# Kernel optimization log

Measured on AMD Instinct MI355X. Metric: run time of the kernel, lower is better.

The kernel has to match this reference:

```python
import jax, jax.numpy as jnp
import numpy as np

B, L, D, T, S, K = 16, 4095, 768, 768, 64, 8
H = T // 2  # per-direction GRU hidden


def setup_inputs() -> dict:
    key = jax.random.key(0)
    ks = jax.random.split(key, 16)
    sc = 0.05
    hidden = jax.random.normal(ks[0], (B, L, D), jnp.float32)
    attn_len = jax.random.randint(ks[1], (B,), L // 2, L).astype(jnp.int32)
    span_start = jax.random.randint(ks[2], (B, S), 0, L - 16).astype(jnp.int32)
    span_len = jax.random.randint(ks[3], (B, S), 1, 9).astype(jnp.int32)
    return dict(
        hidden=hidden,
        W_ih_f=jax.random.normal(ks[4], (3 * H, D)) * sc,
        W_hh_f=jax.random.normal(ks[5], (3 * H, H)) * sc,
        b_ih_f=jax.random.normal(ks[6], (3 * H,)) * sc,
        b_hh_f=jax.random.normal(ks[7], (3 * H,)) * sc,
        W_ih_b=jax.random.normal(ks[8], (3 * H, D)) * sc,
        W_hh_b=jax.random.normal(ks[9], (3 * H, H)) * sc,
        b_ih_b=jax.random.normal(ks[10], (3 * H,)) * sc,
        b_hh_b=jax.random.normal(ks[11], (3 * H,)) * sc,
        W_ctx=jax.random.normal(ks[12], (T, D)) * sc,
        b_ctx=jax.random.normal(ks[13], (T,)) * sc,
        W_find=jax.random.normal(ks[14], (1, 2 * T)) * sc,
        attn_len=attn_len,
        span_start=span_start,
        span_len=span_len,
    )


def _gru_dir(x, W_ih, W_hh, b_ih, b_hh, reverse):
    # x: [B, S, D] -> [B, S, H]; torch GRU gate order: r, z, n
    def step(h, xt):
        gi = xt @ W_ih.T + b_ih            # [B, 3H]
        gh = h @ W_hh.T + b_hh
        ir, iz, inn = jnp.split(gi, 3, axis=-1)
        hr, hz, hn = jnp.split(gh, 3, axis=-1)
        r = jax.nn.sigmoid(ir + hr)
        z = jax.nn.sigmoid(iz + hz)
        n = jnp.tanh(inn + r * hn)
        h_new = (1.0 - z) * n + z * h
        return h_new, h_new
    xs = jnp.swapaxes(x, 0, 1)             # [S, B, D]
    h0 = jnp.zeros((x.shape[0], W_hh.shape[1]), x.dtype)
    _, ys = jax.lax.scan(step, h0, xs, reverse=reverse)
    return jnp.swapaxes(ys, 0, 1)          # [B, S, H]


def reference(hidden, W_ih_f, W_hh_f, b_ih_f, b_hh_f, W_ih_b, W_hh_b, b_ih_b, b_hh_b,
              W_ctx, b_ctx, W_find, attn_len, span_start, span_len):
    pos = jnp.arange(L)
    # --- per-span mean pooling (ragged spans, vectorized via masks) ---
    end = span_start + span_len - 1        # inclusive end, as hidden[start:end+1]
    mask = (pos[None, None, :] >= span_start[..., None]) & (pos[None, None, :] <= end[..., None])
    maskf = mask.astype(hidden.dtype)      # [B, S, L]
    cnt = maskf.sum(-1, keepdims=True)
    span_rep = jnp.einsum('bsl,bld->bsd', maskf, hidden) / cnt   # [B, S, D]
    # --- bidirectional GRU over the span sequence ---
    h_f = _gru_dir(span_rep, W_ih_f, W_hh_f, b_ih_f, b_hh_f, reverse=False)
    h_b = _gru_dir(span_rep, W_ih_b, W_hh_b, b_ih_b, b_hh_b, reverse=True)
    rep_ac = jnp.concatenate([h_f, h_b], axis=-1)                # [B, S, T]
    # --- context: mean over valid tokens excluding the last valid token, then linear ---
    n_ctx = (attn_len - 1).astype(hidden.dtype)                  # [B]
    ctx_mask = (pos[None, :] < (attn_len - 1)[:, None]).astype(hidden.dtype)
    ctx = jnp.einsum('bl,bld->bd', ctx_mask, hidden) / n_ctx[:, None]
    rep_context = ctx @ W_ctx.T + b_ctx                          # [B, T]
    # --- findm attention: concat + linear(no bias) + sigmoid + topk + gather ---
    all_reps = jnp.concatenate([rep_ac, rep_context[:, None, :]], axis=1)  # [B, S+1, T]
    wq, wk = W_find[0, :T], W_find[0, T:]
    # sigmoid(W [q; k]) = sigmoid(q.wq + k.wk)
    score = jax.nn.sigmoid((rep_ac @ wq)[:, :, None] + (all_reps @ wk)[:, None, :])  # [B, S, S+1]
    vals, idx = jax.lax.top_k(score, K)                          # [B, S, K]
    v1 = jnp.take_along_axis(all_reps[:, None, :, :], idx[..., None], axis=2)        # [B, S, K, T]
    return rep_ac, rep_context, v1, vals, idx
```

## Files before the change

kernel.cpp:

```cpp
#include <hip/hip_runtime.h>
#include <hip/hip_bf16.h>
#include <math.h>

#define BB 16
#define LL 4095
#define DD 768
#define TT 768
#define SS 64
#define KK 8
#define HH 384
#define G3 1152
#define NWPD 24

__global__ void span_mean_kernel(const float* __restrict__ hidden,
                                 const int* __restrict__ sstart,
                                 const int* __restrict__ slen,
                                 float* __restrict__ span) {
    int bs = blockIdx.x;
    int b = bs >> 6;
    int st = sstart[bs];
    int ln = slen[bs];
    const float* base = hidden + ((size_t)b * LL + st) * DD;
    float inv = 1.0f / (float)ln;
    for (int d = threadIdx.x; d < DD; d += 256) {
        float acc = 0.0f;
        for (int r = 0; r < ln; ++r) acc += base[(size_t)r * DD + d];
        span[(size_t)bs * DD + d] = acc * inv;
    }
}

__global__ void ctx_accum_kernel(const float* __restrict__ hidden,
                                 const int* __restrict__ attn_len,
                                 float* __restrict__ ctx) {
    int b = blockIdx.x, chunk = blockIdx.y;
    int lim = attn_len[b] - 1;
    int l0 = chunk * 128;
    int l1 = min(l0 + 128, lim);
    if (l0 >= l1) return;
    int t = threadIdx.x;
    const float* base = hidden + (size_t)b * LL * DD;
    float a0 = 0.f, a1 = 0.f, a2 = 0.f;
    for (int l = l0; l < l1; ++l) {
        const float* row = base + (size_t)l * DD;
        a0 += row[t]; a1 += row[t + 256]; a2 += row[t + 512];
    }
    atomicAdd(&ctx[b * DD + t], a0);
    atomicAdd(&ctx[b * DD + t + 256], a1);
    atomicAdd(&ctx[b * DD + t + 512], a2);
}

__global__ void repctx_kernel(const float* __restrict__ ctxsum,
                              const int* __restrict__ attn_len,
                              const float* __restrict__ W_ctx,
                              const float* __restrict__ b_ctx,
                              float* __restrict__ out_rc) {
    int b = blockIdx.x;
    int j = blockIdx.y * 256 + threadIdx.x;
    __shared__ float cv[DD];
    float inv = 1.0f / (float)(attn_len[b] - 1);
    for (int d = threadIdx.x; d < DD; d += 256) cv[d] = ctxsum[b * DD + d] * inv;
    __syncthreads();
    const float* wr = W_ctx + (size_t)j * DD;
    float acc = b_ctx[j];
    for (int d = 0; d < DD; ++d) acc += wr[d] * cv[d];
    out_rc[b * TT + j] = acc;
}

__global__ __launch_bounds__(256) void gi_gemm_kernel(
        const float* __restrict__ span,
        const float* __restrict__ Wf, const float* __restrict__ Wb,
        const float* __restrict__ bihf, const float* __restrict__ bhhf,
        const float* __restrict__ bihb, const float* __restrict__ bhhb,
        float* __restrict__ gi) {
    int dir = blockIdx.z;
    const float* W = dir ? Wb : Wf;
    const float* bih = dir ? bihb : bihf;
    const float* bhh = dir ? bhhb : bhhf;
    int m0 = blockIdx.x * 64, n0 = blockIdx.y * 64;
    __shared__ float As[64][17];
    __shared__ float Bs[64][17];
    int t = threadIdx.x, tx = t & 15, ty = t >> 4;
    float acc[4][4] = {{0.f}};
    for (int k0 = 0; k0 < DD; k0 += 16) {
        for (int e = t; e < 1024; e += 256) {
            int r = e >> 4, c = e & 15;
            As[r][c] = span[(size_t)(m0 + r) * DD + k0 + c];
            Bs[r][c] = W[(size_t)(n0 + r) * DD + k0 + c];
        }
        __syncthreads();
#pragma unroll
        for (int kk = 0; kk < 16; ++kk) {
            float a[4], bv[4];
#pragma unroll
            for (int i = 0; i < 4; ++i) a[i] = As[ty * 4 + i][kk];
#pragma unroll
            for (int j = 0; j < 4; ++j) bv[j] = Bs[tx * 4 + j][kk];
#pragma unroll
            for (int i = 0; i < 4; ++i)
#pragma unroll
                for (int j = 0; j < 4; ++j) acc[i][j] += a[i] * bv[j];
        }
        __syncthreads();
    }
#pragma unroll
    for (int i = 0; i < 4; ++i)
#pragma unroll
        for (int j = 0; j < 4; ++j) {
            int m = m0 + ty * 4 + i, n = n0 + tx * 4 + j;
            float v = acc[i][j] + bih[n] + (n < 2 * HH ? bhh[n] : 0.0f);
            gi[((size_t)dir * 1024 + m) * G3 + n] = v;
        }
}

__global__ __launch_bounds__(256, 1) void scan_coop_kernel(
        const float* __restrict__ gi,
        const float* __restrict__ Whf, const float* __restrict__ Whb,
        const float* __restrict__ bhhf, const float* __restrict__ bhhb,
        unsigned long long* __restrict__ hpair,
        float* __restrict__ repac) {
    int wg = blockIdx.x;
    int dir = wg / NWPD;
    int w = wg % NWPD;
    int t = threadIdx.x;
    int kseg = t & 15, i_loc = t >> 4;
    int i_glob = w * 16 + i_loc;
    const float* Wh = dir ? Whb : Whf;

    float4 wr[3][6];
#pragma unroll
    for (int g = 0; g < 3; ++g)
#pragma unroll
        for (int j = 0; j < 6; ++j) {
            wr[g][j] = *(const float4*)(Wh + (size_t)(g * HH + i_glob) * HH + kseg * 4 + 64 * j);
            asm volatile("" : "+v"(wr[g][j].x), "+v"(wr[g][j].y),
                              "+v"(wr[g][j].z), "+v"(wr[g][j].w));
        }
    float bhn = (dir ? bhhb : bhhf)[2 * HH + i_glob];

    __shared__ __align__(16) float hs[6144];
    float4* hs4 = (float4*)hs;

    for (int s = 0; s < 64; ++s) {
        int p = dir ? (63 - s) : s;
        const float* grow = gi + ((size_t)dir * 1024 + kseg * 64 + p) * G3;
        float g_r = grow[i_glob], g_z = grow[HH + i_glob], g_n = grow[2 * HH + i_glob];
        {
            const unsigned long long* src = hpair + (size_t)((s & 1) * 2 + dir) * 6144;
            unsigned int expect = (unsigned int)s;
            unsigned long long vals[24];
            for (;;) {
                bool ok = true;
#pragma unroll
                for (int j = 0; j < 24; ++j) {
                    vals[j] = __hip_atomic_load(src + j * 256 + t,
                                                __ATOMIC_RELAXED, __HIP_MEMORY_SCOPE_AGENT);
                    ok &= ((unsigned int)(vals[j] >> 32) == expect);
                }
                if (ok) break;
                __builtin_amdgcn_s_sleep(1);
            }
#pragma unroll
            for (int j = 0; j < 24; ++j)
                hs[j * 256 + t] = __uint_as_float((unsigned int)vals[j]);
        }
        __syncthreads();
        float pr[16], pz[16], pn[16];
#pragma unroll
        for (int b = 0; b < 16; ++b) {
            float4 hq[6];
#pragma unroll
            for (int j = 0; j < 6; ++j) hq[j] = hs4[b * 96 + kseg + 16 * j];
            float ar = 0.f, az = 0.f, an = 0.f;
#pragma unroll
            for (int j = 0; j < 6; ++j) {
                ar += wr[0][j].x * hq[j].x + wr[0][j].y * hq[j].y + wr[0][j].z * hq[j].z + wr[0][j].w * hq[j].w;
                az += wr[1][j].x * hq[j].x + wr[1][j].y * hq[j].y + wr[1][j].z * hq[j].z + wr[1][j].w * hq[j].w;
                an += wr[2][j].x * hq[j].x + wr[2][j].y * hq[j].y + wr[2][j].z * hq[j].z + wr[2][j].w * hq[j].w;
            }
            pr[b] = ar; pz[b] = az; pn[b] = an;
        }
        float qr[8], qz[8], qn[8];
        {
            const bool hi = (kseg & 8) != 0;
#pragma unroll
            for (int j = 0; j < 8; ++j) {
                float sr_ = hi ? pr[j] : pr[j + 8];
                qr[j] = (hi ? pr[j + 8] : pr[j]) + __shfl_xor(sr_, 8);
                float sz_ = hi ? pz[j] : pz[j + 8];
                qz[j] = (hi ? pz[j + 8] : pz[j]) + __shfl_xor(sz_, 8);
                float sn_ = hi ? pn[j] : pn[j + 8];
                qn[j] = (hi ? pn[j + 8] : pn[j]) + __shfl_xor(sn_, 8);
            }
        }
        float ur[4], uz[4], un[4];
        {
            const bool hi = (kseg & 4) != 0;
#pragma unroll
            for (int j = 0; j < 4; ++j) {
                float sr_ = hi ? qr[j] : qr[j + 4];
                ur[j] = (hi ? qr[j + 4] : qr[j]) + __shfl_xor(sr_, 4);
                float sz_ = hi ? qz[j] : qz[j + 4];
                uz[j] = (hi ? qz[j + 4] : qz[j]) + __shfl_xor(sz_, 4);
                float sn_ = hi ? qn[j] : qn[j + 4];
                un[j] = (hi ? qn[j + 4] : qn[j]) + __shfl_xor(sn_, 4);
            }
        }
        float vr[2], vz[2], vn[2];
        {
            const bool hi = (kseg & 2) != 0;
#pragma unroll
            for (int j = 0; j < 2; ++j) {
                float sr_ = hi ? ur[j] : ur[j + 2];
                vr[j] = (hi ? ur[j + 2] : ur[j]) + __shfl_xor(sr_, 2);
                float sz_ = hi ? uz[j] : uz[j + 2];
                vz[j] = (hi ? uz[j + 2] : uz[j]) + __shfl_xor(sz_, 2);
                float sn_ = hi ? un[j] : un[j + 2];
                vn[j] = (hi ? un[j + 2] : un[j]) + __shfl_xor(sn_, 2);
            }
        }
        float sr, sz, sn;
        {
            const bool hi = (kseg & 1) != 0;
            float sr_ = hi ? vr[0] : vr[1];
            sr = (hi ? vr[1] : vr[0]) + __shfl_xor(sr_, 1);
            float sz_ = hi ? vz[0] : vz[1];
            sz = (hi ? vz[1] : vz[0]) + __shfl_xor(sz_, 1);
            float sn_ = hi ? vn[0] : vn[1];
            sn = (hi ? vn[1] : vn[0]) + __shfl_xor(sn_, 1);
        }
        float r = 1.0f / (1.0f + expf(-(g_r + sr)));
        float z = 1.0f / (1.0f + expf(-(g_z + sz)));
        float n = tanhf(g_n + r * (sn + bhn));
        float hold = hs[kseg * 384 + i_glob];
        float hnew = (1.0f - z) * n + z * hold;
        unsigned long long pv = ((unsigned long long)(unsigned int)(s + 1) << 32)
                              | (unsigned long long)__float_as_uint(hnew);
        __hip_atomic_store(hpair + (size_t)(((s + 1) & 1) * 2 + dir) * 6144 + kseg * 384 + i_glob,
                           pv, __ATOMIC_RELAXED, __HIP_MEMORY_SCOPE_AGENT);
        repac[(size_t)(kseg * 64 + p) * TT + dir * HH + i_glob] = hnew;
        __syncthreads();
    }
}

__global__ void qkv_kernel(const float* __restrict__ repac,
                           const float* __restrict__ repctx,
                           const float* __restrict__ Wfind,
                           float* __restrict__ qv, float* __restrict__ kv) {
    int w = blockIdx.x * 4 + (threadIdx.x >> 6);
    int lane = threadIdx.x & 63;
    const float* row;
    const float* vec;
    float* dst;
    if (w < 1024) {
        row = repac + (size_t)w * TT;
        vec = Wfind;
        dst = qv + w;
    } else {
        int u = w - 1024;
        int b = u / 65, j = u % 65;
        row = (j < 64) ? (repac + (size_t)(b * 64 + j) * TT) : (repctx + (size_t)b * TT);
        vec = Wfind + TT;
        dst = kv + u;
    }
    double acc = 0.0;
    for (int d = lane; d < TT; d += 64) acc += (double)row[d] * (double)vec[d];
#pragma unroll
    for (int off = 32; off > 0; off >>= 1) acc += __shfl_down(acc, off);
    if (lane == 0) *dst = (float)acc;
}

__global__ void topk_kernel(const float* __restrict__ qv,
                            const float* __restrict__ kv,
                            float* __restrict__ vals_out,
                            float* __restrict__ idx_out,
                            int* __restrict__ idxw) {
    int t = threadIdx.x;
    int bs = blockIdx.x * 256 + t;
    int b = bs >> 6;
    int b0 = (blockIdx.x * 256) >> 6;
    __shared__ float kvs[4 * 65];
    for (int e = t; e < 4 * 65; e += 256) kvs[e] = kv[(b0 + e / 65) * 65 + e % 65];
    __syncthreads();
    const float* myk = kvs + (b - b0) * 65;
    float q = qv[bs];
    float sc[65];
#pragma unroll 1
    for (int j = 0; j < 65; ++j) {
        float x = q + myk[j];
        float e = (float)exp(-(double)x);
        sc[j] = 1.0f / (1.0f + e);
    }
    unsigned long long taken = 0ull;
    bool tk64 = false;
    for (int kk = 0; kk < 8; ++kk) {
        float best = -3.0e38f;
        int bj = 0;
        for (int j = 0; j < 65; ++j) {
            bool tkn = (j < 64) ? (((taken >> j) & 1ull) != 0ull) : tk64;
            float v = sc[j];
            if (!tkn && v > best) { best = v; bj = j; }
        }
        if (bj < 64) taken |= (1ull << bj); else tk64 = true;
        vals_out[bs * 8 + kk] = best;
        idx_out[bs * 8 + kk] = (float)bj;
        idxw[bs * 8 + kk] = bj;
    }
}

__global__ void v1_kernel(const float* __restrict__ repac,
                          const float* __restrict__ repctx,
                          const int* __restrict__ idxw,
                          float* __restrict__ v1) {
    int bs = blockIdx.x;
    int b = bs >> 6;
    int t = threadIdx.x;
    for (int kk = 0; kk < 8; ++kk) {
        int j = idxw[bs * 8 + kk];
        const float* src = (j < 64) ? (repac + (size_t)(b * 64 + j) * TT)
                                    : (repctx + (size_t)b * TT);
        float* dst = v1 + ((size_t)bs * 8 + kk) * TT;
        for (int d = t; d < DD; d += 256) dst[d] = src[d];
    }
}

extern "C" void kernel_launch(void* const* d_in, const int* in_sizes, int n_in,
                              void* d_out, int out_size, void* d_ws, size_t ws_size,
                              hipStream_t stream) {
    const float* hidden    = (const float*)d_in[0];
    const float* W_ih_f    = (const float*)d_in[1];
    const float* W_hh_f    = (const float*)d_in[2];
    const float* b_ih_f    = (const float*)d_in[3];
    const float* b_hh_f    = (const float*)d_in[4];
    const float* W_ih_b    = (const float*)d_in[5];
    const float* W_hh_b    = (const float*)d_in[6];
    const float* b_ih_b    = (const float*)d_in[7];
    const float* b_hh_b    = (const float*)d_in[8];
    const float* W_ctx     = (const float*)d_in[9];
    const float* b_ctx     = (const float*)d_in[10];
    const float* W_find    = (const float*)d_in[11];
    const int*   attn_len  = (const int*)d_in[12];
    const int*   span_start= (const int*)d_in[13];
    const int*   span_len  = (const int*)d_in[14];
    (void)in_sizes; (void)n_in; (void)out_size; (void)ws_size;

    float* ws   = (float*)d_ws;
    float* span = ws;
    float* gi   = span + 786432;
    float* ctx  = gi + 2359296;
    float* qv   = ctx + 12288;
    float* kv   = qv + 1024;
    int*   idxw = (int*)(kv + 1040);
    unsigned long long* hpair = (unsigned long long*)span;

    float* out      = (float*)d_out;
    float* o_repac  = out;
    float* o_repctx = out + 786432;
    float* o_v1     = out + 798720;
    float* o_vals   = out + 7090176;
    float* o_idx    = out + 7098368;

    hipMemsetAsync(ctx, 0, (size_t)BB * DD * sizeof(float), stream);

    span_mean_kernel<<<1024, 256, 0, stream>>>(hidden, span_start, span_len, span);
    ctx_accum_kernel<<<dim3(BB, 32), 256, 0, stream>>>(hidden, attn_len, ctx);
    repctx_kernel<<<dim3(BB, 3), 256, 0, stream>>>(ctx, attn_len, W_ctx, b_ctx, o_repctx);
    gi_gemm_kernel<<<dim3(16, 18, 2), 256, 0, stream>>>(span, W_ih_f, W_ih_b,
                                                        b_ih_f, b_hh_f, b_ih_b, b_hh_b, gi);
    hipMemsetAsync(hpair, 0, (size_t)24576 * sizeof(unsigned long long), stream);
    scan_coop_kernel<<<48, 256, 0, stream>>>(gi, W_hh_f, W_hh_b, b_hh_f, b_hh_b,
                                             hpair, o_repac);
    qkv_kernel<<<516, 256, 0, stream>>>(o_repac, o_repctx, W_find, qv, kv);
    topk_kernel<<<4, 256, 0, stream>>>(qv, kv, o_vals, o_idx, idxw);
    v1_kernel<<<1024, 256, 0, stream>>>(o_repac, o_repctx, idxw, o_v1);
}
```

Measured before the change: 947.8 us.

## Vectorize span mean and v1 copy, transpose GEMM smem tiles, unroll topk

The span-mean and v1 gather kernels now move data as float4 instead of scalar floats, cutting the number of memory instructions. The gi GEMM stores its shared tiles k-major so each thread fetches its 4 A and 4 B values with one float4 shared load each. The topk kernel runs one 64-thread block per batch instead of four 256-thread blocks, and its loops are fully unrolled so the score array can stay in registers. The scan kernel dominates total time, so these edits only touch the smaller stages, and the transposed tile writes may cause shared-memory bank conflicts.

```diff
diff --git a/kernel.cpp b/kernel.cpp
--- a/kernel.cpp
+++ b/kernel.cpp
@@ -20,12 +20,16 @@
     int b = bs >> 6;
     int st = sstart[bs];
     int ln = slen[bs];
-    const float* base = hidden + ((size_t)b * LL + st) * DD;
+    const float4* base = (const float4*)(hidden + ((size_t)b * LL + st) * DD);
+    float4* dst = (float4*)(span + (size_t)bs * DD);
     float inv = 1.0f / (float)ln;
-    for (int d = threadIdx.x; d < DD; d += 256) {
-        float acc = 0.0f;
-        for (int r = 0; r < ln; ++r) acc += base[(size_t)r * DD + d];
-        span[(size_t)bs * DD + d] = acc * inv;
+    for (int d = threadIdx.x; d < DD / 4; d += 256) {
+        float4 acc = make_float4(0.f, 0.f, 0.f, 0.f);
+        for (int r = 0; r < ln; ++r) {
+            float4 v = base[(size_t)r * (DD / 4) + d];
+            acc.x += v.x; acc.y += v.y; acc.z += v.z; acc.w += v.w;
+        }
+        dst[d] = make_float4(acc.x * inv, acc.y * inv, acc.z * inv, acc.w * inv);
     }
 }
 
@@ -77,24 +81,23 @@
     const float* bih = dir ? bihb : bihf;
     const float* bhh = dir ? bhhb : bhhf;
     int m0 = blockIdx.x * 64, n0 = blockIdx.y * 64;
-    __shared__ float As[64][17];
-    __shared__ float Bs[64][17];
+    __shared__ float As[16][68];
+    __shared__ float Bs[16][68];
     int t = threadIdx.x, tx = t & 15, ty = t >> 4;
     float acc[4][4] = {{0.f}};
     for (int k0 = 0; k0 < DD; k0 += 16) {
         for (int e = t; e < 1024; e += 256) {
             int r = e >> 4, c = e & 15;
-            As[r][c] = span[(size_t)(m0 + r) * DD + k0 + c];
-            Bs[r][c] = W[(size_t)(n0 + r) * DD + k0 + c];
+            As[c][r] = span[(size_t)(m0 + r) * DD + k0 + c];
+            Bs[c][r] = W[(size_t)(n0 + r) * DD + k0 + c];
         }
         __syncthreads();
 #pragma unroll
         for (int kk = 0; kk < 16; ++kk) {
-            float a[4], bv[4];
-#pragma unroll
-            for (int i = 0; i < 4; ++i) a[i] = As[ty * 4 + i][kk];
-#pragma unroll
-            for (int j = 0; j < 4; ++j) bv[j] = Bs[tx * 4 + j][kk];
+            float4 a4 = *(const float4*)&As[kk][ty * 4];
+            float4 b4 = *(const float4*)&Bs[kk][tx * 4];
+            float a[4] = {a4.x, a4.y, a4.z, a4.w};
+            float bv[4] = {b4.x, b4.y, b4.z, b4.w};
 #pragma unroll
             for (int i = 0; i < 4; ++i)
 #pragma unroll
@@ -269,24 +272,23 @@
     if (lane == 0) *dst = (float)acc;
 }
 
-__global__ void topk_kernel(const float* __restrict__ qv,
+__global__ __launch_bounds__(64) void topk_kernel(
+                            const float* __restrict__ qv,
                             const float* __restrict__ kv,
                             float* __restrict__ vals_out,
                             float* __restrict__ idx_out,
                             int* __restrict__ idxw) {
     int t = threadIdx.x;
-    int bs = blockIdx.x * 256 + t;
-    int b = bs >> 6;
-    int b0 = (blockIdx.x * 256) >> 6;
-    __shared__ float kvs[4 * 65];
-    for (int e = t; e < 4 * 65; e += 256) kvs[e] = kv[(b0 + e / 65) * 65 + e % 65];
+    int b = blockIdx.x;
+    int bs = b * 64 + t;
+    __shared__ float kvs[65];
+    for (int e = t; e < 65; e += 64) kvs[e] = kv[b * 65 + e];
     __syncthreads();
-    const float* myk = kvs + (b - b0) * 65;
     float q = qv[bs];
     float sc[65];
-#pragma unroll 1
+#pragma unroll
     for (int j = 0; j < 65; ++j) {
-        float x = q + myk[j];
+        float x = q + kvs[j];
         float e = (float)exp(-(double)x);
         sc[j] = 1.0f / (1.0f + e);
     }
@@ -295,6 +297,7 @@
     for (int kk = 0; kk < 8; ++kk) {
         float best = -3.0e38f;
         int bj = 0;
+#pragma unroll
         for (int j = 0; j < 65; ++j) {
             bool tkn = (j < 64) ? (((taken >> j) & 1ull) != 0ull) : tk64;
             float v = sc[j];
@@ -316,10 +319,10 @@
     int t = threadIdx.x;
     for (int kk = 0; kk < 8; ++kk) {
         int j = idxw[bs * 8 + kk];
-        const float* src = (j < 64) ? (repac + (size_t)(b * 64 + j) * TT)
-                                    : (repctx + (size_t)b * TT);
-        float* dst = v1 + ((size_t)bs * 8 + kk) * TT;
-        for (int d = t; d < DD; d += 256) dst[d] = src[d];
+        const float4* src = (const float4*)((j < 64) ? (repac + (size_t)(b * 64 + j) * TT)
+                                                     : (repctx + (size_t)b * TT));
+        float4* dst = (float4*)(v1 + ((size_t)bs * 8 + kk) * TT);
+        for (int d = t; d < DD / 4; d += 256) dst[d] = src[d];
     }
 }
 
@@ -370,6 +373,6 @@
     scan_coop_kernel<<<48, 256, 0, stream>>>(gi, W_hh_f, W_hh_b, b_hh_f, b_hh_b,
                                              hpair, o_repac);
     qkv_kernel<<<516, 256, 0, stream>>>(o_repac, o_repctx, W_find, qv, kv);
-    topk_kernel<<<4, 256, 0, stream>>>(qv, kv, o_vals, o_idx, idxw);
+    topk_kernel<<<16, 64, 0, stream>>>(qv, kv, o_vals, o_idx, idxw);
     v1_kernel<<<1024, 256, 0, stream>>>(o_repac, o_repctx, idxw, o_v1);
 }
```

After: 905.1 us. 1.05x faster.
